# Optimization experiments

Hardware: AMD Instinct MI355X
Metric: run time of the kernel (lower is better)

## Reference

```python
import jax, jax.numpy as jnp
import numpy as np

B, L, D, H, A = 4, 2048, 1024, 16, 64  # batch, seq, d_model, n_head, d_head


def setup_inputs() -> dict:
    key = jax.random.key(0)
    ks = jax.random.split(key, 6)
    scale = 1.0 / np.sqrt(D)
    return {
        "xq": jax.random.normal(ks[0], (B, L, D), dtype=jnp.float32),
        "xkv": jax.random.normal(ks[1], (B, L, D), dtype=jnp.float32),
        "Q": jax.random.normal(ks[2], (D, H, A), dtype=jnp.float32) * scale,
        "K": jax.random.normal(ks[3], (D, H, A), dtype=jnp.float32) * scale,
        "V": jax.random.normal(ks[4], (D, H, A), dtype=jnp.float32) * scale,
        "O": jax.random.normal(ks[5], (D, H, A), dtype=jnp.float32) * scale,
    }


def reference(xq, xkv, Q, K, V, O):
    # embed: 'dha, ...ld -> ...lha'
    q = jnp.einsum('dha,bld->blha', Q, xq)
    k = jnp.einsum('dha,bld->blha', K, xkv)
    v = jnp.einsum('dha,bld->blha', V, xkv)
    # outer: '...lha, ...mha -> ...hlm'  (full LxL score matrix, no scaling in source)
    scores = jnp.einsum('blha,bmha->bhlm', q, k)
    attn = jax.nn.softmax(scores, axis=-1)  # dropout p=0 (eval)
    # score: '...hlm, ...mha -> ...lha'
    ctx = jnp.einsum('bhlm,bmha->blha', attn, v)
    # output: '...dha, ...lha -> ...ld'
    return jnp.einsum('dha,blha->bld', O, ctx)
```

## Files before the change

### kernel.cpp

```cpp
#include <hip/hip_runtime.h>
#include <math.h>

typedef __bf16 bf16;
typedef bf16 bf16x8 __attribute__((ext_vector_type(8)));
typedef bf16 bf16x4 __attribute__((ext_vector_type(4)));
typedef float f32x4 __attribute__((ext_vector_type(4)));
typedef float f32x16 __attribute__((ext_vector_type(16)));

#define B_ 4
#define L_ 2048
#define D_ 1024
#define H_ 16
#define A_ 64
#define HA_ 1024
#define BL_ 8192
#define LOG2E 1.44269504088896340736f

__device__ __forceinline__ void gload16(const void* g, void* l) {
  __builtin_amdgcn_global_load_lds((const __attribute__((address_space(1))) void*)g,
                                   (__attribute__((address_space(3))) void*)l,
                                   16, 0, 0);
}

__device__ __forceinline__ unsigned cvt_pk_bf16(float lo, float hi) {
  unsigned r;
  asm volatile("v_cvt_pk_bf16_f32 %0, %1, %2" : "=v"(r) : "v"(lo), "v"(hi));
  return r;
}

__device__ __forceinline__ void permswap(unsigned& a, unsigned& b) {
  asm volatile("v_permlane32_swap_b32 %0, %1" : "+v"(a), "+v"(b));
}

__global__ __launch_bounds__(256) void cast_f32_bf16(const float* __restrict__ src,
                                                     bf16* __restrict__ dst, int n8) {
  int i = blockIdx.x * blockDim.x + threadIdx.x;
  if (i >= n8) return;
  const float4* s = reinterpret_cast<const float4*>(src) + (size_t)i * 2;
  float4 a = s[0], b = s[1];
  bf16x8 o;
  o[0] = (bf16)a.x; o[1] = (bf16)a.y; o[2] = (bf16)a.z; o[3] = (bf16)a.w;
  o[4] = (bf16)b.x; o[5] = (bf16)b.y; o[6] = (bf16)b.z; o[7] = (bf16)b.w;
  *reinterpret_cast<bf16x8*>(dst + (size_t)i * 8) = o;
}

__global__ __launch_bounds__(256) void transpose_cast_w3(const float* __restrict__ wq,
                                                         const float* __restrict__ wk,
                                                         const float* __restrict__ wv,
                                                         bf16* __restrict__ oq,
                                                         bf16* __restrict__ ok,
                                                         bf16* __restrict__ ov) {
  __shared__ float tile[32][33];
  const int z = blockIdx.z;
  const float* w = (z == 0) ? wq : (z == 1) ? wk : wv;
  bf16* wt = (z == 0) ? oq : (z == 1) ? ok : ov;
  const float scale = (z == 0) ? LOG2E : 1.0f;
  const int d0 = blockIdx.y * 32, h0 = blockIdx.x * 32;
  const int tx = threadIdx.x, ty = threadIdx.y;
  #pragma unroll
  for (int j = 0; j < 4; j++)
    tile[ty + j * 8][tx] = w[(size_t)(d0 + ty + j * 8) * HA_ + h0 + tx];
  __syncthreads();
  #pragma unroll
  for (int j = 0; j < 4; j++)
    wt[(size_t)(h0 + ty + j * 8) * D_ + d0 + tx] = (bf16)(tile[tx][ty + j * 8] * scale);
}

__global__ __launch_bounds__(256) void transpose_v(const bf16* __restrict__ vb,
                                                   bf16* __restrict__ vtb) {
  __shared__ bf16 tile[64][72];
  const int bh = blockIdx.y;
  const int l0 = blockIdx.x * 64;
  const bf16* src = vb + (size_t)bh * L_ * A_ + (size_t)l0 * A_;
  bf16* dst = vtb + (size_t)bh * A_ * L_ + l0;
  const int tid = threadIdx.x;
  {
    int r = tid >> 2, cs = (tid & 3) * 16;
    bf16x8 v0 = *reinterpret_cast<const bf16x8*>(src + r * 64 + cs);
    bf16x8 v1 = *reinterpret_cast<const bf16x8*>(src + r * 64 + cs + 8);
    #pragma unroll
    for (int j = 0; j < 8; j++) { tile[r][cs + j] = v0[j]; tile[r][cs + 8 + j] = v1[j]; }
  }
  __syncthreads();
  {
    int a = tid >> 2, ls = (tid & 3) * 16;
    bf16x8 o0, o1;
    #pragma unroll
    for (int j = 0; j < 8; j++) { o0[j] = tile[ls + j][a]; o1[j] = tile[ls + 8 + j][a]; }
    *reinterpret_cast<bf16x8*>(dst + (size_t)a * L_ + ls) = o0;
    *reinterpret_cast<bf16x8*>(dst + (size_t)a * L_ + ls + 8) = o1;
  }
}

template <int MODE>
__device__ __forceinline__ void gemm_bt_core(const bf16* __restrict__ Ap,
                                             const bf16* __restrict__ Bp,
                                             void* __restrict__ Cp) {
  const int K = 1024;
  __shared__ __align__(16) bf16 As[128 * 32];
  __shared__ __align__(16) bf16 Bs[128 * 32];
  const int tid = threadIdx.x;
  const int m0 = blockIdx.x * 128, n0 = blockIdx.y * 128;
  const int lane = tid & 63, w = tid >> 6;
  const int wr = w >> 1, wc = w & 1;
  const int g = lane >> 4, c = lane & 15;
  f32x4 acc[4][4] = {};
  const int srow = tid >> 2, sch = tid & 3;
  const int sw0 = (sch ^ (srow & 3)) * 8;
  for (int k0 = 0; k0 < K; k0 += 32) {
    gload16(Ap + (size_t)(m0 + srow) * K + k0 + sw0, As + tid * 8);
    gload16(Ap + (size_t)(m0 + 64 + srow) * K + k0 + sw0, As + (256 + tid) * 8);
    gload16(Bp + (size_t)(n0 + srow) * K + k0 + sw0, Bs + tid * 8);
    gload16(Bp + (size_t)(n0 + 64 + srow) * K + k0 + sw0, Bs + (256 + tid) * 8);
    __syncthreads();
    bf16x8 af[4], bfr[4];
    #pragma unroll
    for (int m = 0; m < 4; m++)
      af[m] = *reinterpret_cast<const bf16x8*>(As + (wr * 64 + m * 16 + c) * 32 + ((g ^ (c & 3)) * 8));
    #pragma unroll
    for (int n = 0; n < 4; n++)
      bfr[n] = *reinterpret_cast<const bf16x8*>(Bs + (wc * 64 + n * 16 + c) * 32 + ((g ^ (c & 3)) * 8));
    #pragma unroll
    for (int m = 0; m < 4; m++)
      #pragma unroll
      for (int n = 0; n < 4; n++)
        acc[m][n] = __builtin_amdgcn_mfma_f32_16x16x32_bf16(af[m], bfr[n], acc[m][n], 0, 0, 0);
    __syncthreads();
  }
  #pragma unroll
  for (int m = 0; m < 4; m++) {
    #pragma unroll
    for (int n = 0; n < 4; n++) {
      #pragma unroll
      for (int i = 0; i < 4; i++) {
        int row = m0 + wr * 64 + m * 16 + g * 4 + i;
        int col = n0 + wc * 64 + n * 16 + c;
        float v = acc[m][n][i];
        if (MODE == 0) {
          int b = row >> 11, l = row & 2047, h = col >> 6, a = col & 63;
          ((bf16*)Cp)[(((size_t)b * H_ + h) * L_ + l) * A_ + a] = (bf16)v;
        } else {
          ((float*)Cp)[(size_t)row * 1024 + col] = v;
        }
      }
    }
  }
}

__global__ __launch_bounds__(256, 2) void gemm_proj(const bf16* xq_b, const bf16* xkv_b,
                                                    const bf16* wq, const bf16* wk, const bf16* wv,
                                                    bf16* qb, bf16* kb, bf16* vb) {
  const int z = blockIdx.z;
  const bf16* Ap = (z == 0) ? xq_b : xkv_b;
  const bf16* Bp = (z == 0) ? wq : (z == 1) ? wk : wv;
  bf16* Cp = (z == 0) ? qb : (z == 1) ? kb : vb;
  gemm_bt_core<0>(Ap, Bp, Cp);
}

__global__ __launch_bounds__(256, 2) void gemm_out_k(const bf16* ctx, const bf16* wo, float* out) {
  gemm_bt_core<1>(ctx, wo, out);
}

__device__ __forceinline__ void pa_build(const f32x16& s, bf16x8& f0, bf16x8& f1) {
  #pragma unroll
  for (int sl = 0; sl < 2; sl++) {
    unsigned a0 = cvt_pk_bf16(s[8 * sl + 0], s[8 * sl + 1]);
    unsigned b0 = cvt_pk_bf16(s[8 * sl + 4], s[8 * sl + 5]);
    permswap(a0, b0);
    unsigned a1 = cvt_pk_bf16(s[8 * sl + 2], s[8 * sl + 3]);
    unsigned b1 = cvt_pk_bf16(s[8 * sl + 6], s[8 * sl + 7]);
    permswap(a1, b1);
    uint4 v; v.x = a0; v.y = a1; v.z = b0; v.w = b1;
    if (sl == 0) f0 = __builtin_bit_cast(bf16x8, v);
    else         f1 = __builtin_bit_cast(bf16x8, v);
  }
}

__global__ __launch_bounds__(512, 2) void attn_kernel(const bf16* __restrict__ qg,
                                                      const bf16* __restrict__ kg,
                                                      const bf16* __restrict__ vtg,
                                                      bf16* __restrict__ ctx) {
  __shared__ __align__(16) bf16 Ks[2][64 * 64];
  __shared__ __align__(16) bf16 Vs[2][64 * 64];
  const int tid = threadIdx.x;
  const int lane = tid & 63;
  const int w = tid >> 6;
  const int c = lane & 31;
  const int hi = lane >> 5;
  const int cs7 = c & 7;
  const int bh = blockIdx.x;
  const int q0 = blockIdx.y * 256;
  const bf16* qh = qg + (size_t)bh * L_ * A_;
  const bf16* kh = kg + (size_t)bh * L_ * A_;
  const bf16* vh = vtg + (size_t)bh * A_ * L_;

  const int qrow = q0 + w * 32 + c;
  bf16x8 qf[4];
  #pragma unroll
  for (int ds = 0; ds < 4; ds++)
    qf[ds] = *reinterpret_cast<const bf16x8*>(qh + (size_t)qrow * A_ + ds * 16 + hi * 8);

  bf16x8 ones;
  #pragma unroll
  for (int j = 0; j < 8; j++) ones[j] = (bf16)1.0f;

  f32x16 oacc0 = {}, oacc1 = {};
  f32x16 ssum = {};

  int koA[4], koB[4];
  #pragma unroll
  for (int ds = 0; ds < 4; ds++) {
    koA[ds] = c * 64 + ((2 * ds + hi) ^ cs7) * 8;
    koB[ds] = (32 + c) * 64 + ((2 * ds + hi) ^ cs7) * 8;
  }

  const int sr = tid >> 3, sc = tid & 7;
  const int ss = (sc ^ (sr & 7)) * 8;
  const bf16* ksrc = kh + (size_t)sr * A_ + ss;
  const bf16* vsrc = vh + (size_t)sr * L_ + ss;

  gload16(ksrc, &Ks[0][tid * 8]);
  gload16(vsrc, &Vs[0][tid * 8]);
  __syncthreads();
  int cur = 0;

  for (int t = 0; t < L_ / 64; t++) {
    if (t < L_ / 64 - 1) {
      gload16(ksrc + (size_t)(t + 1) * 4096, &Ks[cur ^ 1][tid * 8]);
      gload16(vsrc + (size_t)(t + 1) * 64, &Vs[cur ^ 1][tid * 8]);
    }
    const bf16* Kc = Ks[cur];
    const bf16* Vc = Vs[cur];

    f32x16 s0 = {}, s1 = {};
    __builtin_amdgcn_s_setprio(1);
    #pragma unroll
    for (int ds = 0; ds < 4; ds++) {
      bf16x8 k0 = *reinterpret_cast<const bf16x8*>(Kc + koA[ds]);
      bf16x8 k1 = *reinterpret_cast<const bf16x8*>(Kc + koB[ds]);
      s0 = __builtin_amdgcn_mfma_f32_32x32x16_bf16(k0, qf[ds], s0, 0, 0, 0);
      s1 = __builtin_amdgcn_mfma_f32_32x32x16_bf16(k1, qf[ds], s1, 0, 0, 0);
    }
    __builtin_amdgcn_s_setprio(0);

    #pragma unroll
    for (int r = 0; r < 16; r++) {
      s0[r] = __builtin_amdgcn_exp2f(s0[r]);
      s1[r] = __builtin_amdgcn_exp2f(s1[r]);
    }

    bf16x8 paf0, paf1, paf2, paf3;
    pa_build(s0, paf0, paf1);
    pa_build(s1, paf2, paf3);

    __builtin_amdgcn_s_setprio(1);
    #pragma unroll
    for (int ks = 0; ks < 4; ks++) {
      const bf16x8 pa = (ks == 0) ? paf0 : (ks == 1) ? paf1 : (ks == 2) ? paf2 : paf3;
      bf16x8 v0 = *reinterpret_cast<const bf16x8*>(Vc + koA[ks]);
      bf16x8 v1 = *reinterpret_cast<const bf16x8*>(Vc + koB[ks]);
      oacc0 = __builtin_amdgcn_mfma_f32_32x32x16_bf16(v0, pa, oacc0, 0, 0, 0);
      oacc1 = __builtin_amdgcn_mfma_f32_32x32x16_bf16(v1, pa, oacc1, 0, 0, 0);
      ssum = __builtin_amdgcn_mfma_f32_32x32x16_bf16(ones, pa, ssum, 0, 0, 0);
    }
    __builtin_amdgcn_s_setprio(0);

    __syncthreads();
    cur ^= 1;
  }

  float inv = 1.f / ssum[0];
  const int b = bh >> 4, h = bh & 15;
  bf16* crow = ctx + (((size_t)b * L_ + qrow) * H_ + h) * A_;
  #pragma unroll
  for (int n = 0; n < 2; n++) {
    #pragma unroll
    for (int rq = 0; rq < 4; rq++) {
      bf16x4 o4;
      #pragma unroll
      for (int j = 0; j < 4; j++) {
        float v = (n == 0) ? oacc0[rq * 4 + j] : oacc1[rq * 4 + j];
        o4[j] = (bf16)(v * inv);
      }
      *reinterpret_cast<bf16x4*>(crow + n * 32 + rq * 8 + hi * 4) = o4;
    }
  }
}

extern "C" void kernel_launch(void* const* d_in, const int* in_sizes, int n_in,
                              void* d_out, int out_size, void* d_ws, size_t ws_size,
                              hipStream_t stream) {
  const float* xq = (const float*)d_in[0];
  const float* xkv = (const float*)d_in[1];
  const float* Qw = (const float*)d_in[2];
  const float* Kw = (const float*)d_in[3];
  const float* Vw = (const float*)d_in[4];
  const float* Ow = (const float*)d_in[5];
  float* out = (float*)d_out;

  char* ws = (char*)d_ws;
  const size_t SZ16 = (size_t)BL_ * HA_ * sizeof(bf16);
  const size_t SZW = (size_t)D_ * HA_ * sizeof(bf16);
  bf16* xq_b = (bf16*)(ws);
  bf16* xkv_b = (bf16*)(ws + SZ16);
  bf16* wq_t = (bf16*)(ws + 2 * SZ16);
  bf16* wk_t = (bf16*)(ws + 2 * SZ16 + SZW);
  bf16* wv_t = (bf16*)(ws + 2 * SZ16 + 2 * SZW);
  bf16* wo_b = (bf16*)(ws + 2 * SZ16 + 3 * SZW);
  bf16* qb = (bf16*)(ws + 2 * SZ16 + 4 * SZW);
  bf16* kb = qb + (size_t)BL_ * HA_;
  bf16* vb = kb + (size_t)BL_ * HA_;
  bf16* vtb = xq_b;
  bf16* ctxb = xkv_b;

  cast_f32_bf16<<<4096, 256, 0, stream>>>(xq, xq_b, BL_ * D_ / 8);
  cast_f32_bf16<<<4096, 256, 0, stream>>>(xkv, xkv_b, BL_ * D_ / 8);
  cast_f32_bf16<<<512, 256, 0, stream>>>(Ow, wo_b, D_ * HA_ / 8);
  transpose_cast_w3<<<dim3(32, 32, 3), dim3(32, 8), 0, stream>>>(Qw, Kw, Vw, wq_t, wk_t, wv_t);

  gemm_proj<<<dim3(64, 8, 3), 256, 0, stream>>>(xq_b, xkv_b, wq_t, wk_t, wv_t, qb, kb, vb);
  transpose_v<<<dim3(32, 64), 256, 0, stream>>>(vb, vtb);
  attn_kernel<<<dim3(64, 8), 512, 0, stream>>>(qb, kb, vtb, ctxb);
  gemm_out_k<<<dim3(64, 8), 256, 0, stream>>>(ctxb, wo_b, out);
}
```

Before: 203.6 us.

## Fuse V transpose into projection GEMM, merge casts, swizzle blocks, drop sum MFMA

Several independent changes. The V projection GEMM now writes its output directly in transposed [bh][a][l] layout, which removes the separate transpose_v kernel and its round trip through memory. The three cast launches are merged into one. Both GEMMs get an XCD-aware block-to-tile mapping meant to improve L2 reuse. In attention, the row sum is computed with VALU adds plus a permlane swap instead of an extra ones-vector MFMA per step. The transposed V stores are 8-byte bf16x4 writes strided by L, which may coalesce less well than before.

```diff
diff --git a/kernel.cpp b/kernel.cpp
--- a/kernel.cpp
+++ b/kernel.cpp
@@ -32,16 +32,36 @@
   asm volatile("v_permlane32_swap_b32 %0, %1" : "+v"(a), "+v"(b));
 }
 
-__global__ __launch_bounds__(256) void cast_f32_bf16(const float* __restrict__ src,
-                                                     bf16* __restrict__ dst, int n8) {
+__device__ __forceinline__ void half_pair(float x, float& o1, float& o2) {
+  unsigned a = __builtin_bit_cast(unsigned, x), b;
+  asm volatile("v_mov_b32 %0, %1" : "=v"(b) : "v"(a));
+  asm volatile("v_permlane32_swap_b32 %0, %1" : "+v"(a), "+v"(b));
+  o1 = __builtin_bit_cast(float, a);
+  o2 = __builtin_bit_cast(float, b);
+}
+
+__global__ __launch_bounds__(256) void cast_all(const float* __restrict__ xq,
+                                                const float* __restrict__ xkv,
+                                                const float* __restrict__ ow,
+                                                bf16* __restrict__ xq_b,
+                                                bf16* __restrict__ xkv_b,
+                                                bf16* __restrict__ wo_b) {
+  const int NX = BL_ * D_ / 8;
+  const int NW = D_ * HA_ / 8;
   int i = blockIdx.x * blockDim.x + threadIdx.x;
-  if (i >= n8) return;
-  const float4* s = reinterpret_cast<const float4*>(src) + (size_t)i * 2;
+  const float* src;
+  bf16* dst;
+  int j;
+  if (i < NX) { src = xq; dst = xq_b; j = i; }
+  else if (i < 2 * NX) { src = xkv; dst = xkv_b; j = i - NX; }
+  else if (i < 2 * NX + NW) { src = ow; dst = wo_b; j = i - 2 * NX; }
+  else return;
+  const float4* s = reinterpret_cast<const float4*>(src) + (size_t)j * 2;
   float4 a = s[0], b = s[1];
   bf16x8 o;
   o[0] = (bf16)a.x; o[1] = (bf16)a.y; o[2] = (bf16)a.z; o[3] = (bf16)a.w;
   o[4] = (bf16)b.x; o[5] = (bf16)b.y; o[6] = (bf16)b.z; o[7] = (bf16)b.w;
-  *reinterpret_cast<bf16x8*>(dst + (size_t)i * 8) = o;
+  *reinterpret_cast<bf16x8*>(dst + (size_t)j * 8) = o;
 }
 
 __global__ __launch_bounds__(256) void transpose_cast_w3(const float* __restrict__ wq,
@@ -66,41 +86,15 @@
     wt[(size_t)(h0 + ty + j * 8) * D_ + d0 + tx] = (bf16)(tile[tx][ty + j * 8] * scale);
 }
 
-__global__ __launch_bounds__(256) void transpose_v(const bf16* __restrict__ vb,
-                                                   bf16* __restrict__ vtb) {
-  __shared__ bf16 tile[64][72];
-  const int bh = blockIdx.y;
-  const int l0 = blockIdx.x * 64;
-  const bf16* src = vb + (size_t)bh * L_ * A_ + (size_t)l0 * A_;
-  bf16* dst = vtb + (size_t)bh * A_ * L_ + l0;
-  const int tid = threadIdx.x;
-  {
-    int r = tid >> 2, cs = (tid & 3) * 16;
-    bf16x8 v0 = *reinterpret_cast<const bf16x8*>(src + r * 64 + cs);
-    bf16x8 v1 = *reinterpret_cast<const bf16x8*>(src + r * 64 + cs + 8);
-    #pragma unroll
-    for (int j = 0; j < 8; j++) { tile[r][cs + j] = v0[j]; tile[r][cs + 8 + j] = v1[j]; }
-  }
-  __syncthreads();
-  {
-    int a = tid >> 2, ls = (tid & 3) * 16;
-    bf16x8 o0, o1;
-    #pragma unroll
-    for (int j = 0; j < 8; j++) { o0[j] = tile[ls + j][a]; o1[j] = tile[ls + 8 + j][a]; }
-    *reinterpret_cast<bf16x8*>(dst + (size_t)a * L_ + ls) = o0;
-    *reinterpret_cast<bf16x8*>(dst + (size_t)a * L_ + ls + 8) = o1;
-  }
-}
-
 template <int MODE>
 __device__ __forceinline__ void gemm_bt_core(const bf16* __restrict__ Ap,
                                              const bf16* __restrict__ Bp,
-                                             void* __restrict__ Cp) {
+                                             void* __restrict__ Cp,
+                                             int m0, int n0) {
   const int K = 1024;
   __shared__ __align__(16) bf16 As[128 * 32];
   __shared__ __align__(16) bf16 Bs[128 * 32];
   const int tid = threadIdx.x;
-  const int m0 = blockIdx.x * 128, n0 = blockIdx.y * 128;
   const int lane = tid & 63, w = tid >> 6;
   const int wr = w >> 1, wc = w & 1;
   const int g = lane >> 4, c = lane & 15;
@@ -131,34 +125,53 @@
   for (int m = 0; m < 4; m++) {
     #pragma unroll
     for (int n = 0; n < 4; n++) {
-      #pragma unroll
-      for (int i = 0; i < 4; i++) {
-        int row = m0 + wr * 64 + m * 16 + g * 4 + i;
+      if (MODE == 2) {
+        int row0 = m0 + wr * 64 + m * 16 + g * 4;
         int col = n0 + wc * 64 + n * 16 + c;
-        float v = acc[m][n][i];
-        if (MODE == 0) {
-          int b = row >> 11, l = row & 2047, h = col >> 6, a = col & 63;
-          ((bf16*)Cp)[(((size_t)b * H_ + h) * L_ + l) * A_ + a] = (bf16)v;
-        } else {
-          ((float*)Cp)[(size_t)row * 1024 + col] = v;
+        int b = row0 >> 11, l0 = row0 & 2047, h = col >> 6, a = col & 63;
+        bf16x4 o4;
+        #pragma unroll
+        for (int i = 0; i < 4; i++) o4[i] = (bf16)acc[m][n][i];
+        *reinterpret_cast<bf16x4*>((bf16*)Cp + ((size_t)(b * H_ + h) * A_ + a) * L_ + l0) = o4;
+      } else {
+        #pragma unroll
+        for (int i = 0; i < 4; i++) {
+          int row = m0 + wr * 64 + m * 16 + g * 4 + i;
+          int col = n0 + wc * 64 + n * 16 + c;
+          float v = acc[m][n][i];
+          if (MODE == 0) {
+            int b = row >> 11, l = row & 2047, h = col >> 6, a = col & 63;
+            ((bf16*)Cp)[(((size_t)b * H_ + h) * L_ + l) * A_ + a] = (bf16)v;
+          } else {
+            ((float*)Cp)[(size_t)row * 1024 + col] = v;
+          }
         }
       }
     }
   }
 }
 
+__device__ __forceinline__ void xcd_mn(int id, int& m0, int& n0) {
+  int xcd = id & 7, j = id >> 3;
+  m0 = (xcd * 8 + (j >> 3)) * 128;
+  n0 = (j & 7) * 128;
+}
+
 __global__ __launch_bounds__(256, 2) void gemm_proj(const bf16* xq_b, const bf16* xkv_b,
                                                     const bf16* wq, const bf16* wk, const bf16* wv,
-                                                    bf16* qb, bf16* kb, bf16* vb) {
+                                                    bf16* qb, bf16* kb, bf16* vtb) {
+  int m0, n0;
+  xcd_mn(blockIdx.x, m0, n0);
   const int z = blockIdx.z;
-  const bf16* Ap = (z == 0) ? xq_b : xkv_b;
-  const bf16* Bp = (z == 0) ? wq : (z == 1) ? wk : wv;
-  bf16* Cp = (z == 0) ? qb : (z == 1) ? kb : vb;
-  gemm_bt_core<0>(Ap, Bp, Cp);
+  if (z == 0)      gemm_bt_core<0>(xq_b, wq, qb, m0, n0);
+  else if (z == 1) gemm_bt_core<0>(xkv_b, wk, kb, m0, n0);
+  else             gemm_bt_core<2>(xkv_b, wv, vtb, m0, n0);
 }
 
 __global__ __launch_bounds__(256, 2) void gemm_out_k(const bf16* ctx, const bf16* wo, float* out) {
-  gemm_bt_core<1>(ctx, wo, out);
+  int m0, n0;
+  xcd_mn(blockIdx.x, m0, n0);
+  gemm_bt_core<1>(ctx, wo, out, m0, n0);
 }
 
 __device__ __forceinline__ void pa_build(const f32x16& s, bf16x8& f0, bf16x8& f1) {
@@ -200,12 +213,8 @@
   for (int ds = 0; ds < 4; ds++)
     qf[ds] = *reinterpret_cast<const bf16x8*>(qh + (size_t)qrow * A_ + ds * 16 + hi * 8);
 
-  bf16x8 ones;
-  #pragma unroll
-  for (int j = 0; j < 8; j++) ones[j] = (bf16)1.0f;
-
   f32x16 oacc0 = {}, oacc1 = {};
-  f32x16 ssum = {};
+  float lrun = 0.f;
 
   int koA[4], koB[4];
   #pragma unroll
@@ -248,6 +257,15 @@
       s0[r] = __builtin_amdgcn_exp2f(s0[r]);
       s1[r] = __builtin_amdgcn_exp2f(s1[r]);
     }
+
+    float u0[8];
+    #pragma unroll
+    for (int r = 0; r < 8; r++)
+      u0[r] = (s0[r] + s0[r + 8]) + (s1[r] + s1[r + 8]);
+    float us = ((u0[0] + u0[1]) + (u0[2] + u0[3])) + ((u0[4] + u0[5]) + (u0[6] + u0[7]));
+    float y1, y2;
+    half_pair(us, y1, y2);
+    lrun += y1 + y2;
 
     bf16x8 paf0, paf1, paf2, paf3;
     pa_build(s0, paf0, paf1);
@@ -261,7 +279,6 @@
       bf16x8 v1 = *reinterpret_cast<const bf16x8*>(Vc + koB[ks]);
       oacc0 = __builtin_amdgcn_mfma_f32_32x32x16_bf16(v0, pa, oacc0, 0, 0, 0);
       oacc1 = __builtin_amdgcn_mfma_f32_32x32x16_bf16(v1, pa, oacc1, 0, 0, 0);
-      ssum = __builtin_amdgcn_mfma_f32_32x32x16_bf16(ones, pa, ssum, 0, 0, 0);
     }
     __builtin_amdgcn_s_setprio(0);
 
@@ -269,7 +286,7 @@
     cur ^= 1;
   }
 
-  float inv = 1.f / ssum[0];
+  float inv = 1.f / lrun;
   const int b = bh >> 4, h = bh & 15;
   bf16* crow = ctx + (((size_t)b * L_ + qrow) * H_ + h) * A_;
   #pragma unroll
@@ -309,17 +326,14 @@
   bf16* wo_b = (bf16*)(ws + 2 * SZ16 + 3 * SZW);
   bf16* qb = (bf16*)(ws + 2 * SZ16 + 4 * SZW);
   bf16* kb = qb + (size_t)BL_ * HA_;
-  bf16* vb = kb + (size_t)BL_ * HA_;
-  bf16* vtb = xq_b;
+  bf16* vtb = kb + (size_t)BL_ * HA_;
   bf16* ctxb = xkv_b;
 
-  cast_f32_bf16<<<4096, 256, 0, stream>>>(xq, xq_b, BL_ * D_ / 8);
-  cast_f32_bf16<<<4096, 256, 0, stream>>>(xkv, xkv_b, BL_ * D_ / 8);
-  cast_f32_bf16<<<512, 256, 0, stream>>>(Ow, wo_b, D_ * HA_ / 8);
+  const int NCAST = (2 * BL_ * D_ + D_ * HA_) / 8;
+  cast_all<<<(NCAST + 255) / 256, 256, 0, stream>>>(xq, xkv, Ow, xq_b, xkv_b, wo_b);
   transpose_cast_w3<<<dim3(32, 32, 3), dim3(32, 8), 0, stream>>>(Qw, Kw, Vw, wq_t, wk_t, wv_t);
 
-  gemm_proj<<<dim3(64, 8, 3), 256, 0, stream>>>(xq_b, xkv_b, wq_t, wk_t, wv_t, qb, kb, vb);
-  transpose_v<<<dim3(32, 64), 256, 0, stream>>>(vb, vtb);
+  gemm_proj<<<dim3(512, 1, 3), 256, 0, stream>>>(xq_b, xkv_b, wq_t, wk_t, wv_t, qb, kb, vtb);
   attn_kernel<<<dim3(64, 8), 512, 0, stream>>>(qb, kb, vtb, ctxb);
-  gemm_out_k<<<dim3(64, 8), 256, 0, stream>>>(ctxb, wo_b, out);
-}
+  gemm_out_k<<<512, 256, 0, stream>>>(ctxb, wo_b, out);
+}
```

Result: faster. 192.3 us (-5.5%).
